# Kernel tuning notes

Measured on AMD Instinct MI355X. Metric: run time of the kernel, lower is better.

Reference implementation:

```python
import jax, jax.numpy as jnp
import numpy as np

B, N, L, D = 64, 512, 12, 128   # batch, nodes, neighbors, node_dim==edge_dim
Z = 3 * D                        # 2*node_dim + edge_dim
NC = 3                           # n_convs
VOCAB = 1000
BN_EPS = 1e-3                    # keras BatchNormalization default epsilon


def setup_inputs() -> dict:
    key = jax.random.key(0)
    ks = jax.random.split(key, 14)
    inp = {}
    inp['node_types'] = jax.random.randint(ks[0], (B, N), 0, VOCAB)
    inp['neighbor_list'] = jax.random.randint(ks[1], (B, N, L), 0, N)
    inp['edge_types'] = jax.random.randint(ks[2], (B, N, L), 0, VOCAB)
    inp['slot_types'] = jax.random.normal(ks[3], (B, N, D), jnp.float32)
    inp['node_w'] = jax.random.normal(ks[4], (VOCAB, D), jnp.float32) * 0.1
    inp['edge_w'] = jax.random.normal(ks[5], (VOCAB, D), jnp.float32) * 0.1
    inp['wf'] = jax.random.normal(ks[6], (NC, Z, D), jnp.float32) * 0.05
    inp['bf'] = jax.random.normal(ks[7], (NC, D), jnp.float32) * 0.01
    inp['ws'] = jax.random.normal(ks[8], (NC, Z, D), jnp.float32) * 0.05
    inp['bs'] = jax.random.normal(ks[9], (NC, D), jnp.float32) * 0.01
    inp['bn_gamma'] = jnp.ones((NC, D), jnp.float32)
    inp['bn_beta'] = jnp.zeros((NC, D), jnp.float32)
    inp['bn_mean'] = jax.random.normal(ks[10], (NC, D), jnp.float32) * 0.01
    inp['bn_var'] = jax.random.uniform(ks[11], (NC, D), jnp.float32, 0.5, 1.5)
    inp['dense_w'] = jax.random.normal(ks[12], (D, 1), jnp.float32) * 0.1
    inp['dense_b'] = jnp.zeros((1,), jnp.float32)
    return inp


def _embed(w, x):
    # gather with negative-index masking, as in Embedding.call (inference path)
    idx = jnp.where(x < 0, 0, x)
    mask = (x >= 0).astype(jnp.float32)[..., None]
    return w[idx] * mask


def reference(node_types, neighbor_list, edge_types, slot_types,
              node_w, edge_w, wf, bf, ws, bs,
              bn_gamma, bn_beta, bn_mean, bn_var, dense_w, dense_b):
    v = _embed(node_w, node_types) + slot_types          # (B, N, D)
    e = _embed(edge_w, edge_types)                       # (B, N, L, D)

    nl = neighbor_list
    n_safe = jnp.where(nl < 0, 0, nl)                    # (B, N, L)
    nmask = (nl >= 0).astype(jnp.float32)[..., None]     # (B, N, L, 1)

    for i in range(NC):
        # neighbor gather: per-batch index into node axis
        nn = jax.vmap(lambda vv, ii: vv[ii])(v, n_safe) * nmask  # (B, N, L, D)
        v_view = jnp.broadcast_to(v[:, :, None, :], nn.shape)
        z = jnp.concatenate([v_view, nn, e], axis=-1)            # (B, N, L, Z)
        s = (jax.nn.sigmoid(jnp.einsum('bnlz,zd->bnld', z, wf[i]) + bf[i])
             * jnp.tanh(jnp.einsum('bnlz,zd->bnld', z, ws[i]) + bs[i])
             * nmask)
        v_next = v + jnp.sum(s, axis=2)                          # (B, N, D)

        # masked batchnorm (inference: moving stats); invalid rows -> 0
        vf = v_next.reshape(-1, D)
        valid = jnp.all(jnp.abs(vf) > 1e-5, axis=-1)
        bn = bn_gamma[i] * (vf - bn_mean[i]) * jax.lax.rsqrt(bn_var[i] + BN_EPS) + bn_beta[i]
        v = jnp.where(valid[:, None], bn, 0.0).reshape(B, N, D)

    # masked mean pooling over nodes
    pmask = (node_types >= 0).astype(jnp.float32)[..., None]     # (B, N, 1)
    pooled = jnp.sum(v * pmask, axis=1) / jnp.sum(pmask, axis=1)  # (B, D)
    return pooled @ dense_w + dense_b                            # (B, 1)
```

## Files before the change

### kernel.cpp

```cpp
#include <hip/hip_runtime.h>

#define NB 64
#define NN 512
#define NL 12
#define ND 128
#define NZ 384
#define NCONV 3
#define VOCAB 1000
#define BN_EPS 1e-3f
#define LO_SCALE 2048.0f
#define INV_LO (1.0f/2048.0f)
#define SCF (-1.4426950408889634f)
#define SCS ( 2.8853900817779268f)

typedef _Float16 f16;
using half8 = __attribute__((ext_vector_type(8))) _Float16;
using floatx16 = __attribute__((ext_vector_type(16))) float;

__device__ __forceinline__ floatx16 mfma32(half8 a, half8 b, floatx16 c) {
    return __builtin_amdgcn_mfma_f32_32x32x16_f16(a, b, c, 0, 0, 0);
}
__device__ __forceinline__ void split1(float x, f16& h, f16& l) {
    h = (f16)x; l = (f16)((x - (float)h) * LO_SCALE);
}

__global__ __launch_bounds__(256) void prep_kernel(
    const float* __restrict__ wf, const float* __restrict__ wsg,
    f16* __restrict__ Wc_hi, f16* __restrict__ Wc_lo)
{
    int id = blockIdx.x * 256 + threadIdx.x;
    int c = id >> 16;
    int rem = id & 65535;
    int col = rem >> 7, k = rem & 127;
    int part = col >> 7;
    int d = col & 127;
    int z = (part < 2) ? (128 + k) : k;
    const float* W = (part & 1) ? wsg : wf;
    float wv = W[((size_t)c * NZ + z) * ND + d];
    f16 h, l; split1(wv, h, l);
    size_t dst = (size_t)c * 65536 + (size_t)(k >> 3) * 4096 + col * 8 + (k & 7);
    Wc_hi[dst] = h; Wc_lo[dst] = l;
}

__global__ __launch_bounds__(256) void ew_kernel(
    const float* __restrict__ edge_w, const float* __restrict__ wf,
    const float* __restrict__ wsg, float* __restrict__ EWp)
{
    __shared__ float se[32][128];
    const int c = blockIdx.x >> 5;
    const int tyg = (blockIdx.x & 31) * 32;
    const int tid = threadIdx.x;
    for (int i = tid; i < 4096; i += 256) {
        int ty = i >> 7, k = i & 127;
        int tyv = tyg + ty;
        se[ty][k] = (tyv < VOCAB) ? edge_w[(size_t)tyv * ND + k] : 0.f;
    }
    __syncthreads();
    const int h = tid >> 7, col = tid & 127;
    const float* W = h ? wsg : wf;
    const float sc = h ? SCS : SCF;
    float acc[32];
    #pragma unroll
    for (int ty = 0; ty < 32; ++ty) acc[ty] = 0.f;
    #pragma unroll 4
    for (int k = 0; k < 128; ++k) {
        float wv = W[((size_t)c * NZ + 256 + k) * ND + col];
        #pragma unroll
        for (int ty = 0; ty < 32; ++ty) acc[ty] = fmaf(se[ty][k], wv, acc[ty]);
    }
    #pragma unroll
    for (int ty = 0; ty < 32; ++ty) {
        int tyv = tyg + ty;
        if (tyv <= VOCAB)
            EWp[(((size_t)c * (VOCAB + 1) + tyv) * 128 + col) * 2 + h] = acc[ty] * sc;
    }
}

__global__ __launch_bounds__(256) void embed_kernel(
    const int* __restrict__ node_types, const float* __restrict__ slot_types,
    const float* __restrict__ node_w, f16* __restrict__ vhi, f16* __restrict__ vlo)
{
    int i = blockIdx.x * 256 + threadIdx.x;
    int bn = i >> 7, d = i & 127;
    int ty = node_types[bn];
    float m = ty >= 0 ? 1.f : 0.f;
    int idx = ty >= 0 ? ty : 0;
    float v = node_w[(size_t)idx * ND + d] * m + slot_types[i];
    f16 h, l; split1(v, h, l);
    vhi[i] = h; vlo[i] = l;
}

__global__ __launch_bounds__(256, 3) void psgemm_kernel(
    const f16* __restrict__ vhi, const f16* __restrict__ vlo,
    const f16* __restrict__ Wc_hi, const f16* __restrict__ Wc_lo,
    const float* __restrict__ bfv, const float* __restrict__ bsv,
    float* __restrict__ Ppk, float* __restrict__ Spk)
{
    __shared__ __align__(16) char sA[16384];
    const int hw = blockIdx.x;
    const int xcd = hw & 7;
    const int q = hw >> 3;
    const int bl = q >> 5;
    const int r = q & 31;
    const int half = r >> 4;
    const int xloc = r & 15;
    const int batch = bl * 8 + xcd;
    const int node0 = batch * NN + xloc * 32;

    const int tid = threadIdx.x;
    const int lane = tid & 63, w = tid >> 6;
    const int l31 = lane & 31, l32 = lane >> 5;

    #pragma unroll
    for (int it = 0; it < 2; ++it) {
        int slot = it * 256 + tid;
        int rr = slot >> 4, cc = slot & 15;
        int cs = cc ^ (rr & 15);
        size_t src = (size_t)(node0 + rr) * ND + cs * 8;
        *(half8*)(sA + rr * 256 + cc * 16) = *(const half8*)(vhi + src);
        *(half8*)(sA + 8192 + rr * 256 + cc * 16) = *(const half8*)(vlo + src);
    }
    __syncthreads();

    const int dcol = w * 32 + l31;
    const int col0 = half * 256 + dcol;
    const int col1 = col0 + 128;

    floatx16 a00 = {}, a10 = {}, a01 = {}, a11 = {};

    int ch0 = l32;
    half8 b0h = *(const half8*)(Wc_hi + (size_t)ch0 * 4096 + col0 * 8);
    half8 b0l = *(const half8*)(Wc_lo + (size_t)ch0 * 4096 + col0 * 8);
    half8 b1h = *(const half8*)(Wc_hi + (size_t)ch0 * 4096 + col1 * 8);
    half8 b1l = *(const half8*)(Wc_lo + (size_t)ch0 * 4096 + col1 * 8);

    #pragma unroll
    for (int ks = 0; ks < 8; ++ks) {
        half8 n0h, n0l, n1h, n1l;
        if (ks < 7) {
            int nch = (ks + 1) * 2 + l32;
            n0h = *(const half8*)(Wc_hi + (size_t)nch * 4096 + col0 * 8);
            n0l = *(const half8*)(Wc_lo + (size_t)nch * 4096 + col0 * 8);
            n1h = *(const half8*)(Wc_hi + (size_t)nch * 4096 + col1 * 8);
            n1l = *(const half8*)(Wc_lo + (size_t)nch * 4096 + col1 * 8);
        }
        int qq = (((ks * 2 + l32) ^ (l31 & 15)) << 4);
        half8 ah = *(const half8*)(sA + l31 * 256 + qq);
        half8 al = *(const half8*)(sA + 8192 + l31 * 256 + qq);
        a00 = mfma32(ah, b0h, a00);
        a10 = mfma32(ah, b0l, a10);
        a10 = mfma32(al, b0h, a10);
        a01 = mfma32(ah, b1h, a01);
        a11 = mfma32(ah, b1l, a11);
        a11 = mfma32(al, b1h, a11);
        b0h = n0h; b0l = n0l; b1h = n1h; b1l = n1l;
    }

    float bx = 0.f, by = 0.f;
    if (half) { bx = bfv[dcol]; by = bsv[dcol]; }
    float* outp = half ? Spk : Ppk;
    #pragma unroll
    for (int rr = 0; rr < 16; ++rr) {
        int orow = (rr & 3) + 8 * (rr >> 2) + 4 * l32;
        float2 v2 = { (a00[rr] + a10[rr] * INV_LO + bx) * SCF,
                      (a01[rr] + a11[rr] * INV_LO + by) * SCS };
        *(float2*)(outp + ((size_t)(node0 + orow) * 128 + dcol) * 2) = v2;
    }
}

__global__ __launch_bounds__(256, 4) void edge_epilogue_kernel(
    f16* __restrict__ vhi, f16* __restrict__ vlo,
    const int* __restrict__ neighbor_list, const int* __restrict__ edge_types,
    const float* __restrict__ Ppk, const float* __restrict__ Spk,
    const float* __restrict__ EWp,
    const float* __restrict__ bn_gamma, const float* __restrict__ bn_beta,
    const float* __restrict__ bn_mean, const float* __restrict__ bn_var)
{
    __shared__ int s_nl[2][12], s_et[2][12];
    __shared__ int s_flags[2][2];
    const int hw = blockIdx.x;
    const int xcd = hw & 7;
    const int q = hw >> 3;
    const int b = (q >> 8) * 8 + xcd;
    const int j = q & 255;
    const int node0 = b * NN + j * 2;

    const int tid = threadIdx.x;
    if (tid < 24) {
        int g = tid >= 12, l = tid - g * 12;
        s_nl[g][l] = neighbor_list[(node0 + g) * NL + l];
        s_et[g][l] = edge_types[(node0 + g) * NL + l];
    }
    __syncthreads();
    const int g = tid >> 7, d = tid & 127;
    const int node = node0 + g;
    const int bbase = b * NN;

    float2 sp2 = *(const float2*)(Spk + ((size_t)node * 128 + d) * 2);
    float2 p2[NL], e2[NL];
    float m[NL];
    #pragma unroll
    for (int l = 0; l < NL; ++l) {
        int nl = s_nl[g][l];
        int et = s_et[g][l];
        int ns = (nl >= 0) ? (bbase + nl) : node;
        int es = (et >= 0) ? et : VOCAB;
        ns = __builtin_amdgcn_readfirstlane(ns);
        es = __builtin_amdgcn_readfirstlane(es);
        m[l] = (nl >= 0) ? 1.f : 0.f;
        p2[l] = *(const float2*)(Ppk + ((size_t)ns * 128 + d) * 2);
        e2[l] = *(const float2*)(EWp + ((size_t)es * 128 + d) * 2);
    }
    float sum = 0.f;
    #pragma unroll
    for (int l = 0; l < NL; ++l) {
        float pf = p2[l].x + sp2.x + e2[l].x;
        float ps = p2[l].y + sp2.y + e2[l].y;
        float sig = __builtin_amdgcn_rcpf(1.f + __builtin_amdgcn_exp2f(pf));
        float th  = fmaf(-2.f, __builtin_amdgcn_rcpf(__builtin_amdgcn_exp2f(ps) + 1.f), 1.f);
        sum = fmaf(sig * th, m[l], sum);
    }

    size_t ix = (size_t)node * ND + d;
    float x = (float)vhi[ix] + (float)vlo[ix] * INV_LO + sum;
    int ok = __all(fabsf(x) > 1e-5f);
    int w2 = (tid >> 6) & 1;
    if ((tid & 63) == 0) s_flags[g][w2] = ok;
    __syncthreads();
    int valid = s_flags[g][0] & s_flags[g][1];
    float gm = bn_gamma[d], be = bn_beta[d], mu = bn_mean[d];
    float rsv = __builtin_amdgcn_rcpf(sqrtf(bn_var[d] + BN_EPS));
    float o = valid ? (gm * (x - mu) * rsv + be) : 0.f;
    f16 h, l2; split1(o, h, l2);
    vhi[ix] = h; vlo[ix] = l2;
}

__global__ __launch_bounds__(256) void pool1_kernel(
    const f16* __restrict__ vhi, const f16* __restrict__ vlo,
    const int* __restrict__ node_types, float* __restrict__ partial)
{
    __shared__ float sbuf[128];
    const int b = blockIdx.x >> 3, chunk = blockIdx.x & 7;
    const int d = threadIdx.x & 127, sub = threadIdx.x >> 7;
    const int n0 = chunk * 64 + sub * 32;
    float sum = 0.f;
    #pragma unroll 4
    for (int i = 0; i < 32; ++i) {
        int n = n0 + i;
        int ty = node_types[b * NN + n];
        float mk = ty >= 0 ? 1.f : 0.f;
        size_t ix = ((size_t)(b * NN + n)) * ND + d;
        sum += ((float)vhi[ix] + (float)vlo[ix] * INV_LO) * mk;
    }
    if (sub == 0) sbuf[d] = sum;
    __syncthreads();
    if (sub == 1) partial[(size_t)blockIdx.x * 128 + d] = sbuf[d] + sum;
}

__global__ __launch_bounds__(128) void pool2_kernel(
    const float* __restrict__ partial, const int* __restrict__ node_types,
    const float* __restrict__ dense_w, const float* __restrict__ dense_b,
    float* __restrict__ out)
{
    __shared__ float s_part[2], s_cnt[2];
    const int b = blockIdx.x;
    const int d = threadIdx.x;
    float sum = 0.f;
    #pragma unroll
    for (int c = 0; c < 8; ++c) sum += partial[(size_t)(b * 8 + c) * 128 + d];
    float cnt = 0.f;
    #pragma unroll
    for (int i = 0; i < 4; ++i)
        cnt += (node_types[b * NN + d + i * 128] >= 0) ? 1.f : 0.f;
    #pragma unroll
    for (int off = 32; off > 0; off >>= 1) cnt += __shfl_xor(cnt, off);
    if ((d & 63) == 0) s_cnt[d >> 6] = cnt;
    __syncthreads();
    float tcnt = s_cnt[0] + s_cnt[1];
    float pv = (sum / tcnt) * dense_w[d];
    #pragma unroll
    for (int off = 32; off > 0; off >>= 1) pv += __shfl_down(pv, off);
    if ((d & 63) == 0) s_part[d >> 6] = pv;
    __syncthreads();
    if (d == 0) out[b] = s_part[0] + s_part[1] + dense_b[0];
}

extern "C" void kernel_launch(void* const* d_in, const int* in_sizes, int n_in,
                              void* d_out, int out_size, void* d_ws, size_t ws_size,
                              hipStream_t stream) {
    const int*   node_types    = (const int*)d_in[0];
    const int*   neighbor_list = (const int*)d_in[1];
    const int*   edge_types    = (const int*)d_in[2];
    const float* slot_types    = (const float*)d_in[3];
    const float* node_w        = (const float*)d_in[4];
    const float* edge_w        = (const float*)d_in[5];
    const float* wf            = (const float*)d_in[6];
    const float* bfv           = (const float*)d_in[7];
    const float* wsg           = (const float*)d_in[8];
    const float* bsv           = (const float*)d_in[9];
    const float* bn_gamma      = (const float*)d_in[10];
    const float* bn_beta       = (const float*)d_in[11];
    const float* bn_mean       = (const float*)d_in[12];
    const float* bn_var        = (const float*)d_in[13];
    const float* dense_w       = (const float*)d_in[14];
    const float* dense_b       = (const float*)d_in[15];
    float* out = (float*)d_out;

    float* wsf = (float*)d_ws;
    float* Ppk = wsf;
    float* Spk = wsf + 8388608;
    float* EWp = wsf + 2 * 8388608;
    float* pp  = EWp + 768768;
    f16* f16b  = (f16*)(pp + 65536);
    f16* vhiA  = f16b;
    f16* vloA  = vhiA + 4194304;
    f16* Wc_hi = vloA + 4194304;
    f16* Wc_lo = Wc_hi + 196608;

    prep_kernel<<<768, 256, 0, stream>>>(wf, wsg, Wc_hi, Wc_lo);
    ew_kernel<<<NCONV * 32, 256, 0, stream>>>(edge_w, wf, wsg, EWp);
    embed_kernel<<<(NB * NN * ND) / 256, 256, 0, stream>>>(node_types, slot_types, node_w, vhiA, vloA);

    for (int c = 0; c < NCONV; ++c) {
        psgemm_kernel<<<2048, 256, 0, stream>>>(
            vhiA, vloA, Wc_hi + (size_t)c * 65536, Wc_lo + (size_t)c * 65536,
            bfv + c * ND, bsv + c * ND, Ppk, Spk);
        edge_epilogue_kernel<<<(NB * NN) / 2, 256, 0, stream>>>(
            vhiA, vloA, neighbor_list, edge_types,
            Ppk, Spk, EWp + (size_t)c * (VOCAB + 1) * 256,
            bn_gamma + c * ND, bn_beta + c * ND, bn_mean + c * ND, bn_var + c * ND);
    }

    pool1_kernel<<<NB * 8, 256, 0, stream>>>(vhiA, vloA, node_types, pp);
    pool2_kernel<<<NB, 128, 0, stream>>>(pp, node_types, dense_w, dense_b, out);
}
```

Before: 289.2 us.

## Map one wave per node in edge epilogue with float4 interleaved P/S/EW layout

Reorders the packed P, S and edge-weight buffers so that each lane reads a float4 holding gate and state pre-activations for two feature columns (d and d+64). The edge epilogue now assigns one 64-lane wave per node instead of 128 threads per node, so shared memory and __syncthreads go away. Neighbor and edge indices are read with readlane and the mask comes from a ballot. The sigmoid*tanh product is folded into a single reciprocal per element, with exponent clamping to avoid overflow. Each thread holds more registers, so the occupancy hint is lowered from 4 to 2.

```diff
diff --git a/kernel.cpp b/kernel.cpp
--- a/kernel.cpp
+++ b/kernel.cpp
@@ -72,7 +72,7 @@
     for (int ty = 0; ty < 32; ++ty) {
         int tyv = tyg + ty;
         if (tyv <= VOCAB)
-            EWp[(((size_t)c * (VOCAB + 1) + tyv) * 128 + col) * 2 + h] = acc[ty] * sc;
+            EWp[((size_t)c * (VOCAB + 1) + tyv) * 256 + (col & 63) * 4 + (col >> 6) * 2 + h] = acc[ty] * sc;
     }
 }
 
@@ -159,16 +159,17 @@
     float bx = 0.f, by = 0.f;
     if (half) { bx = bfv[dcol]; by = bsv[dcol]; }
     float* outp = half ? Spk : Ppk;
+    const int dsub = (dcol & 63) * 4 + (dcol >> 6) * 2;
     #pragma unroll
     for (int rr = 0; rr < 16; ++rr) {
         int orow = (rr & 3) + 8 * (rr >> 2) + 4 * l32;
         float2 v2 = { (a00[rr] + a10[rr] * INV_LO + bx) * SCF,
                       (a01[rr] + a11[rr] * INV_LO + by) * SCS };
-        *(float2*)(outp + ((size_t)(node0 + orow) * 128 + dcol) * 2) = v2;
-    }
-}
-
-__global__ __launch_bounds__(256, 4) void edge_epilogue_kernel(
+        *(float2*)(outp + (size_t)(node0 + orow) * 256 + dsub) = v2;
+    }
+}
+
+__global__ __launch_bounds__(256, 2) void edge_epilogue_kernel(
     f16* __restrict__ vhi, f16* __restrict__ vlo,
     const int* __restrict__ neighbor_list, const int* __restrict__ edge_types,
     const float* __restrict__ Ppk, const float* __restrict__ Spk,
@@ -176,63 +177,70 @@
     const float* __restrict__ bn_gamma, const float* __restrict__ bn_beta,
     const float* __restrict__ bn_mean, const float* __restrict__ bn_var)
 {
-    __shared__ int s_nl[2][12], s_et[2][12];
-    __shared__ int s_flags[2][2];
     const int hw = blockIdx.x;
     const int xcd = hw & 7;
     const int q = hw >> 3;
-    const int b = (q >> 8) * 8 + xcd;
-    const int j = q & 255;
-    const int node0 = b * NN + j * 2;
+    const int b = (q >> 7) * 8 + xcd;
+    const int j = q & 127;
+    const int node0 = b * NN + j * 4;
 
     const int tid = threadIdx.x;
-    if (tid < 24) {
-        int g = tid >= 12, l = tid - g * 12;
-        s_nl[g][l] = neighbor_list[(node0 + g) * NL + l];
-        s_et[g][l] = edge_types[(node0 + g) * NL + l];
-    }
-    __syncthreads();
-    const int g = tid >> 7, d = tid & 127;
-    const int node = node0 + g;
+    const int w = tid >> 6, ds = tid & 63;
+    const int node = node0 + w;
     const int bbase = b * NN;
 
-    float2 sp2 = *(const float2*)(Spk + ((size_t)node * 128 + d) * 2);
-    float2 p2[NL], e2[NL];
-    float m[NL];
+    int nlv = -1, etv = -1;
+    if (ds < NL) {
+        nlv = neighbor_list[node * NL + ds];
+        etv = edge_types[node * NL + ds];
+    }
+    unsigned long long bm = __ballot(nlv >= 0);
+
+    float4 sp4 = *(const float4*)(Spk + (size_t)node * 256 + ds * 4);
+    float4 p4[NL], e4[NL];
     #pragma unroll
     for (int l = 0; l < NL; ++l) {
-        int nl = s_nl[g][l];
-        int et = s_et[g][l];
-        int ns = (nl >= 0) ? (bbase + nl) : node;
-        int es = (et >= 0) ? et : VOCAB;
-        ns = __builtin_amdgcn_readfirstlane(ns);
-        es = __builtin_amdgcn_readfirstlane(es);
-        m[l] = (nl >= 0) ? 1.f : 0.f;
-        p2[l] = *(const float2*)(Ppk + ((size_t)ns * 128 + d) * 2);
-        e2[l] = *(const float2*)(EWp + ((size_t)es * 128 + d) * 2);
-    }
-    float sum = 0.f;
+        int nl_l = __builtin_amdgcn_readlane(nlv, l);
+        int et_l = __builtin_amdgcn_readlane(etv, l);
+        int ns = (nl_l >= 0) ? (bbase + nl_l) : node;
+        int es = (et_l >= 0) ? et_l : VOCAB;
+        p4[l] = *(const float4*)(Ppk + (size_t)ns * 256 + ds * 4);
+        e4[l] = *(const float4*)(EWp + (size_t)es * 256 + ds * 4);
+    }
+
+    float sum0 = 0.f, sum1 = 0.f;
     #pragma unroll
     for (int l = 0; l < NL; ++l) {
-        float pf = p2[l].x + sp2.x + e2[l].x;
-        float ps = p2[l].y + sp2.y + e2[l].y;
-        float sig = __builtin_amdgcn_rcpf(1.f + __builtin_amdgcn_exp2f(pf));
-        float th  = fmaf(-2.f, __builtin_amdgcn_rcpf(__builtin_amdgcn_exp2f(ps) + 1.f), 1.f);
-        sum = fmaf(sig * th, m[l], sum);
-    }
-
-    size_t ix = (size_t)node * ND + d;
-    float x = (float)vhi[ix] + (float)vlo[ix] * INV_LO + sum;
-    int ok = __all(fabsf(x) > 1e-5f);
-    int w2 = (tid >> 6) & 1;
-    if ((tid & 63) == 0) s_flags[g][w2] = ok;
-    __syncthreads();
-    int valid = s_flags[g][0] & s_flags[g][1];
-    float gm = bn_gamma[d], be = bn_beta[d], mu = bn_mean[d];
-    float rsv = __builtin_amdgcn_rcpf(sqrtf(bn_var[d] + BN_EPS));
-    float o = valid ? (gm * (x - mu) * rsv + be) : 0.f;
-    f16 h, l2; split1(o, h, l2);
-    vhi[ix] = h; vlo[ix] = l2;
+        float m = ((bm >> l) & 1) ? 1.f : 0.f;
+        float ax = p4[l].x + sp4.x + e4[l].x;
+        float ay = p4[l].y + sp4.y + e4[l].y;
+        float az = p4[l].z + sp4.z + e4[l].z;
+        float aw = p4[l].w + sp4.w + e4[l].w;
+        float u0 = __builtin_amdgcn_exp2f(fminf(ax, 60.f));
+        float w0 = __builtin_amdgcn_exp2f(fminf(ay, 60.f));
+        float u1 = __builtin_amdgcn_exp2f(fminf(az, 60.f));
+        float w1 = __builtin_amdgcn_exp2f(fminf(aw, 60.f));
+        float r0 = __builtin_amdgcn_rcpf(fmaf(u0, w0, 1.f + u0 + w0));
+        float r1 = __builtin_amdgcn_rcpf(fmaf(u1, w1, 1.f + u1 + w1));
+        sum0 = fmaf((w0 - 1.f) * r0, m, sum0);
+        sum1 = fmaf((w1 - 1.f) * r1, m, sum1);
+    }
+
+    size_t i0 = (size_t)node * ND + ds;
+    size_t i1 = i0 + 64;
+    float x0 = (float)vhi[i0] + (float)vlo[i0] * INV_LO + sum0;
+    float x1 = (float)vhi[i1] + (float)vlo[i1] * INV_LO + sum1;
+    int valid = __all(fabsf(x0) > 1e-5f && fabsf(x1) > 1e-5f);
+
+    float gm0 = bn_gamma[ds], be0 = bn_beta[ds], mu0 = bn_mean[ds];
+    float gm1 = bn_gamma[ds + 64], be1 = bn_beta[ds + 64], mu1 = bn_mean[ds + 64];
+    float rs0 = __builtin_amdgcn_rcpf(sqrtf(bn_var[ds] + BN_EPS));
+    float rs1 = __builtin_amdgcn_rcpf(sqrtf(bn_var[ds + 64] + BN_EPS));
+    float o0 = valid ? (gm0 * (x0 - mu0) * rs0 + be0) : 0.f;
+    float o1 = valid ? (gm1 * (x1 - mu1) * rs1 + be1) : 0.f;
+    f16 h, l2;
+    split1(o0, h, l2); vhi[i0] = h; vlo[i0] = l2;
+    split1(o1, h, l2); vhi[i1] = h; vlo[i1] = l2;
 }
 
 __global__ __launch_bounds__(256) void pool1_kernel(
@@ -325,7 +333,7 @@
         psgemm_kernel<<<2048, 256, 0, stream>>>(
             vhiA, vloA, Wc_hi + (size_t)c * 65536, Wc_lo + (size_t)c * 65536,
             bfv + c * ND, bsv + c * ND, Ppk, Spk);
-        edge_epilogue_kernel<<<(NB * NN) / 2, 256, 0, stream>>>(
+        edge_epilogue_kernel<<<8192, 256, 0, stream>>>(
             vhiA, vloA, neighbor_list, edge_types,
             Ppk, Spk, EWp + (size_t)c * (VOCAB + 1) * 256,
             bn_gamma + c * ND, bn_beta + c * ND, bn_mean + c * ND, bn_var + c * ND);
```

After: 267.9 us. -7.4%, faster.
